# Optimization experiments

Measured on AMD Instinct MI355X. Metric: run time of the kernel, lower is better.

## Reference

```python
import jax, jax.numpy as jnp
import numpy as np

B, IN, H = 8192, 1024, 1024


def setup_inputs() -> dict:
    key = jax.random.key(0)
    ks = jax.random.split(key, 6)
    s = 1.0 / np.sqrt(H)
    return {
        "incoming": jax.random.normal(ks[0], (B, IN), dtype=jnp.float32),
        "state": jax.random.normal(ks[1], (2, B, H), dtype=jnp.float32),
        "Wx": jax.random.normal(ks[2], (4 * H, IN), dtype=jnp.float32) * s,
        "bx": jax.random.normal(ks[3], (4 * H,), dtype=jnp.float32) * s,
        "Wh": jax.random.normal(ks[4], (4 * H, H), dtype=jnp.float32) * s,
        "bh": jax.random.normal(ks[5], (4 * H,), dtype=jnp.float32) * s,
    }


def reference(incoming, state, Wx, bx, Wh, bh):
    # Fused form of 8 Linear layers: gates stacked in (i, f, g, o) order.
    h_prev, c_prev = state[0], state[1]
    gates = (jnp.einsum('bi,gi->bg', incoming, Wx) + bx
             + jnp.einsum('bh,gh->bg', h_prev, Wh) + bh)  # [B, 4H]
    i_g, f_g, g_g, o_g = jnp.split(gates, 4, axis=-1)
    i = jax.nn.sigmoid(i_g)
    f = jax.nn.sigmoid(f_g)
    g = jnp.tanh(g_g)
    o = jax.nn.sigmoid(o_g)
    new_c = f * c_prev + i * g
    new_h = o * jnp.tanh(new_c)
    # output == new_h; return stacked (new_h, new_c) as [2, B, H]
    return jnp.stack([new_h, new_c])
```

## Files before the change

kernel.cpp:

```cpp
#include <hip/hip_runtime.h>
#include <hip/hip_bf16.h>


#define B_DIM 8192
#define H_DIM 1024
#define BH (8192 * 1024)
#define K2 2048

typedef __attribute__((ext_vector_type(4))) float f32x4;
typedef __attribute__((ext_vector_type(8))) __bf16 bf16x8;
typedef __attribute__((ext_vector_type(8))) unsigned short ushort8;

static __device__ __forceinline__ unsigned short f2bf(float f) {
    return __builtin_bit_cast(unsigned short, (__bf16)f);
}
static __device__ __forceinline__ float sigf(float x) {
    return 1.0f / (1.0f + __expf(-x));
}
static __device__ __forceinline__ float tanhft(float x) {
    float e = __expf(2.0f * x);
    return (e - 1.0f) / (e + 1.0f);
}
static __device__ __forceinline__ void gload16(const void* g, void* l) {
    __builtin_amdgcn_global_load_lds(
        (const __attribute__((address_space(1))) unsigned int*)g,
        (__attribute__((address_space(3))) unsigned int*)l, 16, 0, 0);
}
static __device__ __forceinline__ ushort8 cvt8(const float* src) {
    const float4 u = ((const float4*)src)[0];
    const float4 v = ((const float4*)src)[1];
    ushort8 o;
    o[0] = f2bf(u.x); o[1] = f2bf(u.y); o[2] = f2bf(u.z); o[3] = f2bf(u.w);
    o[4] = f2bf(v.x); o[5] = f2bf(v.y); o[6] = f2bf(v.z); o[7] = f2bf(v.w);
    return o;
}

__global__ __launch_bounds__(256) void conv_kernel(
    const float* __restrict__ x, const float* __restrict__ h,
    const float* __restrict__ Wx, const float* __restrict__ Wh,
    unsigned short* __restrict__ A, unsigned short* __restrict__ W)
{
    const int bidx = blockIdx.x;
    if (bidx < 8192) {
        const int id = bidx * 256 + threadIdx.x;
        const int base = id * 8;
        const int b = base >> 11;
        const int k = base & 2047;
        const float* src = (k < 1024) ? (x + (size_t)b * 1024 + k)
                                      : (h + (size_t)b * 1024 + (k - 1024));
        *(ushort8*)(A + base) = cvt8(src);
    } else {
        const int id = (bidx - 8192) * 256 + threadIdx.x;
        const int base = id * 8;
        const int n = base >> 11;
        const int k = base & 2047;
        const int jb = n >> 8, wn = (n >> 6) & 3, g = (n >> 4) & 3, jj = n & 15;
        const int srow = (g << 10) + (jb << 6) + (wn << 4) + jj;
        const float* src = (k < 1024) ? (Wx + (size_t)srow * 1024 + k)
                                      : (Wh + (size_t)srow * 1024 + (k - 1024));
        *(ushort8*)(W + base) = cvt8(src);
    }
}

__global__ __launch_bounds__(512, 2) void lstm_gemm8(
    const unsigned short* __restrict__ Abf, const unsigned short* __restrict__ Wbf,
    const float* __restrict__ bx, const float* __restrict__ bh,
    const float* __restrict__ cprev, float* __restrict__ out)
{
    extern __shared__ unsigned short lds[];

    const int tid = threadIdx.x;
    const int lane = tid & 63;
    const int wv = tid >> 6;
    const int wm = wv >> 2;
    const int wn = wv & 3;
    const int q = lane >> 4, c = lane & 15;

    const int bid = blockIdx.x;
    const int xcd = bid & 7;
    const int idx = bid >> 3;
    const int jb  = xcd * 2 + (idx & 1);
    const int bb  = idx >> 1;
    const int b0 = bb * 256;

    const unsigned short* Ab = Abf + (size_t)b0 * K2;
    const unsigned short* Wb = Wbf + (size_t)(jb * 256) * K2;

    const size_t ssg = (size_t)(tid >> 3) * K2
                     + (size_t)(((tid & 7) ^ ((tid >> 3) & 7)) * 8);
    const unsigned sbase = (unsigned)(tid & 448) * 8;

    const unsigned arow = (unsigned)(wm * 128 + c) * 64;
    const unsigned brow = 16384u + (unsigned)(wn * 64 + c) * 64;
    const unsigned cach = (unsigned)((q ^ (c & 7)) << 3);

    f32x4 acc[8][4];
#pragma unroll
    for (int m = 0; m < 8; ++m)
#pragma unroll
        for (int g = 0; g < 4; ++g) acc[m][g] = f32x4{0.f, 0.f, 0.f, 0.f};

    bf16x8 av[4], bv[4];

#define STG(BUF, ISB, QA, T) do {                                              \
    const unsigned short* _s = (ISB) ? Wb : Ab;                                \
    gload16(_s + ssg + (size_t)(QA) * 64 * K2 + (size_t)((T) & 31) * 64,       \
            &lds[(BUF) * 32768 + (ISB) * 16384 + (QA) * 4096 + sbase]);        \
} while (0)

#define LOADA(BUF, KS, MH) do {                                                \
    const unsigned short* _p = lds + (BUF) * 32768 + (MH) * 4096 + arow        \
                             + (cach ^ ((KS) * 32));                           \
    av[0] = *(const bf16x8*)(_p);                                              \
    av[1] = *(const bf16x8*)(_p + 1024);                                       \
    av[2] = *(const bf16x8*)(_p + 2048);                                       \
    av[3] = *(const bf16x8*)(_p + 3072);                                       \
} while (0)

#define LOADB(BUF, KS) do {                                                    \
    const unsigned short* _p = lds + (BUF) * 32768 + brow                      \
                             + (cach ^ ((KS) * 32));                           \
    bv[0] = *(const bf16x8*)(_p);                                              \
    bv[1] = *(const bf16x8*)(_p + 1024);                                       \
    bv[2] = *(const bf16x8*)(_p + 2048);                                       \
    bv[3] = *(const bf16x8*)(_p + 3072);                                       \
} while (0)

#define MFMA16(MH) do {                                                        \
    __builtin_amdgcn_s_setprio(1);                                             \
    _Pragma("unroll")                                                          \
    for (int _i = 0; _i < 4; ++_i)                                             \
        _Pragma("unroll")                                                      \
        for (int _g = 0; _g < 4; ++_g)                                         \
            acc[(MH) * 4 + _i][_g] = __builtin_amdgcn_mfma_f32_16x16x32_bf16(  \
                av[_i], bv[_g], acc[(MH) * 4 + _i][_g], 0, 0, 0);              \
    __builtin_amdgcn_s_setprio(0);                                             \
} while (0)

#define BAR()    __builtin_amdgcn_s_barrier()
#define WLGKM0() asm volatile("s_waitcnt lgkmcnt(0)")
#define WVM2()   asm volatile("s_waitcnt vmcnt(2)" ::: "memory")

#define TILE(BUF, T1) do {                                                     \
    LOADA(BUF, 0, 0); LOADB(BUF, 0);                                           \
    STG((BUF) ^ 1, 1, 0, T1); STG((BUF) ^ 1, 1, 1, T1);                        \
    BAR(); WLGKM0(); MFMA16(0); WVM2(); BAR();                                 \
    LOADA(BUF, 0, 1);                                                          \
    STG((BUF) ^ 1, 1, 2, T1); STG((BUF) ^ 1, 1, 3, T1);                        \
    BAR(); WLGKM0(); MFMA16(1); BAR();                                         \
    LOADA(BUF, 1, 0); LOADB(BUF, 1);                                           \
    STG((BUF) ^ 1, 0, 0, T1); STG((BUF) ^ 1, 0, 2, T1);                        \
    BAR(); WLGKM0(); MFMA16(0); BAR();                                         \
    LOADA(BUF, 1, 1);                                                          \
    STG((BUF) ^ 1, 0, 1, T1); STG((BUF) ^ 1, 0, 3, T1);                        \
    BAR(); WLGKM0(); MFMA16(1); WVM2(); BAR();                                 \
} while (0)

    STG(0, 1, 0, 0); STG(0, 1, 1, 0); STG(0, 1, 2, 0); STG(0, 1, 3, 0);
    STG(0, 0, 0, 0); STG(0, 0, 2, 0); STG(0, 0, 1, 0); STG(0, 0, 3, 0);
    WVM2();
    BAR();

    for (int u = 0; u < 32; u += 2) {
        TILE(0, u + 1);
        TILE(1, u + 2);
    }

#undef TILE
#undef STG
#undef LOADA
#undef LOADB
#undef MFMA16

    const int j = jb * 64 + wn * 16 + c;
    const float bI = bx[j] + bh[j];
    const float bF = bx[1024 + j] + bh[1024 + j];
    const float bG = bx[2048 + j] + bh[2048 + j];
    const float bO = bx[3072 + j] + bh[3072 + j];
#pragma unroll
    for (int mt = 0; mt < 8; ++mt) {
#pragma unroll
        for (int rr = 0; rr < 4; ++rr) {
            const int row = b0 + wm * 128 + mt * 16 + q * 4 + rr;
            const size_t off = (size_t)row * 1024 + j;
            const float iv = sigf(acc[mt][0][rr] + bI);
            const float fv = sigf(acc[mt][1][rr] + bF);
            const float gv = tanhft(acc[mt][2][rr] + bG);
            const float ov = sigf(acc[mt][3][rr] + bO);
            const float cp = cprev[off];
            const float nc = fv * cp + iv * gv;
            out[off] = ov * tanhft(nc);
            out[BH + off] = nc;
        }
    }
}

__global__ __launch_bounds__(256) void lstm_fallback(
    const float* __restrict__ incoming, const float* __restrict__ state,
    const float* __restrict__ Wx, const float* __restrict__ bx,
    const float* __restrict__ Wh, const float* __restrict__ bh,
    float* __restrict__ out)
{
    __shared__ unsigned short lA[128 * 64];
    __shared__ unsigned short lW[128 * 64];
    const int t = threadIdx.x;
    const int lane = t & 63;
    const int wv = t >> 6;
    const int q = lane >> 4;
    const int c = lane & 15;
    const int j0 = blockIdx.x * 32;
    const int b0 = blockIdx.y * 128;
    const float* hprev = state;
    const float* cprev = state + (size_t)BH;

    f32x4 acc[2][8];
#pragma unroll
    for (int mt = 0; mt < 2; ++mt)
#pragma unroll
        for (int nt = 0; nt < 8; ++nt)
            acc[mt][nt] = f32x4{0.f, 0.f, 0.f, 0.f};

    const int sr = t >> 3;
    const int sk8 = t & 7;

    for (int it = 0; it < 32; ++it) {
        const bool first = (it < 16);
        const float* As = first ? incoming : hprev;
        const float* Ws = first ? Wx : Wh;
        const int kk = first ? it * 64 : it * 64 - 1024;
#pragma unroll
        for (int i = 0; i < 4; ++i) {
            const int r = i * 32 + sr;
            *(ushort8*)&lA[r * 64 + ((sk8 ^ (r & 7)) * 8)] =
                cvt8(As + (size_t)(b0 + r) * 1024 + kk + sk8 * 8);
        }
#pragma unroll
        for (int i = 0; i < 4; ++i) {
            const int n = i * 32 + sr;
            const int grow = ((n >> 5) << 10) + j0 + (n & 31);
            *(ushort8*)&lW[n * 64 + ((sk8 ^ (n & 7)) * 8)] =
                cvt8(Ws + (size_t)grow * 1024 + kk + sk8 * 8);
        }
        __syncthreads();
#pragma unroll
        for (int ks = 0; ks < 2; ++ks) {
            const int k8a = ks * 4 + q;
            bf16x8 av[2], bv[8];
#pragma unroll
            for (int mt = 0; mt < 2; ++mt) {
                const int r = wv * 32 + mt * 16 + c;
                av[mt] = *(const bf16x8*)&lA[r * 64 + ((k8a ^ (r & 7)) * 8)];
            }
#pragma unroll
            for (int nt = 0; nt < 8; ++nt) {
                const int n = nt * 16 + c;
                bv[nt] = *(const bf16x8*)&lW[n * 64 + ((k8a ^ (n & 7)) * 8)];
            }
#pragma unroll
            for (int mt = 0; mt < 2; ++mt)
#pragma unroll
                for (int nt = 0; nt < 8; ++nt)
                    acc[mt][nt] = __builtin_amdgcn_mfma_f32_16x16x32_bf16(
                        av[mt], bv[nt], acc[mt][nt], 0, 0, 0);
        }
        __syncthreads();
    }

    const int b0r = b0 + wv * 32;
#pragma unroll
    for (int jt = 0; jt < 2; ++jt) {
        const int j = j0 + jt * 16 + c;
        const float bI = bx[j] + bh[j];
        const float bF = bx[1024 + j] + bh[1024 + j];
        const float bG = bx[2048 + j] + bh[2048 + j];
        const float bO = bx[3072 + j] + bh[3072 + j];
#pragma unroll
        for (int mt = 0; mt < 2; ++mt) {
#pragma unroll
            for (int rr = 0; rr < 4; ++rr) {
                const int row = b0r + mt * 16 + q * 4 + rr;
                const size_t off = (size_t)row * 1024 + j;
                const float iv = sigf(acc[mt][0 + jt][rr] + bI);
                const float fv = sigf(acc[mt][2 + jt][rr] + bF);
                const float gv = tanhft(acc[mt][4 + jt][rr] + bG);
                const float ov = sigf(acc[mt][6 + jt][rr] + bO);
                const float cp = cprev[off];
                const float nc = fv * cp + iv * gv;
                out[off] = ov * tanhft(nc);
                out[BH + off] = nc;
            }
        }
    }
}

extern "C" void kernel_launch(void* const* d_in, const int* in_sizes, int n_in,
                              void* d_out, int out_size, void* d_ws, size_t ws_size,
                              hipStream_t stream) {
    const float* incoming = (const float*)d_in[0];
    const float* state    = (const float*)d_in[1];
    const float* Wx       = (const float*)d_in[2];
    const float* bx       = (const float*)d_in[3];
    const float* Wh       = (const float*)d_in[4];
    const float* bh       = (const float*)d_in[5];
    float* out = (float*)d_out;

    const float* hprev = state;
    const float* cprev = state + (size_t)BH;

    const size_t A_bytes = (size_t)B_DIM * K2 * 2;
    const size_t W_bytes = (size_t)4 * H_DIM * K2 * 2;

    if (ws_size >= A_bytes + W_bytes) {
        unsigned short* Abf = (unsigned short*)d_ws;
        unsigned short* Wbf = (unsigned short*)((char*)d_ws + A_bytes);
        conv_kernel<<<dim3(12288), dim3(256), 0, stream>>>(
            incoming, hprev, Wx, Wh, Abf, Wbf);
        (void)hipFuncSetAttribute((const void*)lstm_gemm8,
                                  hipFuncAttributeMaxDynamicSharedMemorySize, 131072);
        lstm_gemm8<<<dim3(512), dim3(512), 131072, stream>>>(
            Abf, Wbf, bx, bh, cprev, out);
    } else {
        dim3 grid(H_DIM / 32, B_DIM / 128);
        lstm_fallback<<<grid, dim3(256), 0, stream>>>(
            incoming, state, Wx, bx, Wh, bh, out);
    }
}
```

Before: 159.2 us.

## Restructure LSTM GEMM to 1024-thread blocks with shallower K tiles

The fused bf16 GEMM goes from 512 to 1024 threads per block, and each wave now holds a 64x64 accumulator tile instead of 128x64. The K step shrinks from 64 to 32, which halves LDS use to 64 KB. The four-phase interleaved staging and MFMA schedule is replaced by a simple double-buffered loop that issues the next tile's loads, runs the MFMAs, then waits on all outstanding loads and syncs once per step. This aims for more resident waves and fewer barriers per step. The cost is twice as many K iterations, each with a full vmcnt(0) wait that can expose global-load latency.

Measured after the change: 165.0 us. +3.7%, slower.

```diff
diff --git a/kernel.cpp b/kernel.cpp
--- a/kernel.cpp
+++ b/kernel.cpp
@@ -62,7 +62,7 @@
     }
 }
 
-__global__ __launch_bounds__(512, 2) void lstm_gemm8(
+__global__ __launch_bounds__(1024, 4) void lstm_gemm8(
     const unsigned short* __restrict__ Abf, const unsigned short* __restrict__ Wbf,
     const float* __restrict__ bx, const float* __restrict__ bh,
     const float* __restrict__ cprev, float* __restrict__ out)
@@ -86,90 +86,76 @@
     const unsigned short* Ab = Abf + (size_t)b0 * K2;
     const unsigned short* Wb = Wbf + (size_t)(jb * 256) * K2;
 
-    const size_t ssg = (size_t)(tid >> 3) * K2
-                     + (size_t)(((tid & 7) ^ ((tid >> 3) & 7)) * 8);
-    const unsigned sbase = (unsigned)(tid & 448) * 8;
-
-    const unsigned arow = (unsigned)(wm * 128 + c) * 64;
-    const unsigned brow = 16384u + (unsigned)(wn * 64 + c) * 64;
-    const unsigned cach = (unsigned)((q ^ (c & 7)) << 3);
-
-    f32x4 acc[8][4];
-#pragma unroll
-    for (int m = 0; m < 8; ++m)
+    const size_t ssg = (size_t)(tid >> 2) * K2
+                     + (size_t)(((tid & 3) ^ ((tid >> 3) & 3)) * 8);
+    const unsigned sdst = (unsigned)(tid & 960) * 8;
+
+    const unsigned cq = (unsigned)((q ^ ((c >> 1) & 3)) << 3);
+    const unsigned arow = (unsigned)(wm * 64 + c) * 32 + cq;
+    const unsigned brow = 8192u + (unsigned)(wn * 64 + c) * 32 + cq;
+
+    f32x4 acc[4][4];
+#pragma unroll
+    for (int m = 0; m < 4; ++m)
 #pragma unroll
         for (int g = 0; g < 4; ++g) acc[m][g] = f32x4{0.f, 0.f, 0.f, 0.f};
 
     bf16x8 av[4], bv[4];
 
-#define STG(BUF, ISB, QA, T) do {                                              \
+#define STG(BUF, ISB, T) do {                                                  \
     const unsigned short* _s = (ISB) ? Wb : Ab;                                \
-    gload16(_s + ssg + (size_t)(QA) * 64 * K2 + (size_t)((T) & 31) * 64,       \
-            &lds[(BUF) * 32768 + (ISB) * 16384 + (QA) * 4096 + sbase]);        \
+    gload16(_s + ssg + (size_t)((T) & 63) * 32,                                \
+            &lds[(BUF) * 16384 + (ISB) * 8192 + sdst]);                        \
 } while (0)
 
-#define LOADA(BUF, KS, MH) do {                                                \
-    const unsigned short* _p = lds + (BUF) * 32768 + (MH) * 4096 + arow        \
-                             + (cach ^ ((KS) * 32));                           \
-    av[0] = *(const bf16x8*)(_p);                                              \
-    av[1] = *(const bf16x8*)(_p + 1024);                                       \
-    av[2] = *(const bf16x8*)(_p + 2048);                                       \
-    av[3] = *(const bf16x8*)(_p + 3072);                                       \
+#define RD(BUF) do {                                                           \
+    const unsigned short* _pa = lds + (BUF) * 16384 + arow;                    \
+    const unsigned short* _pb = lds + (BUF) * 16384 + brow;                    \
+    av[0] = *(const bf16x8*)(_pa);                                             \
+    av[1] = *(const bf16x8*)(_pa + 512);                                       \
+    av[2] = *(const bf16x8*)(_pa + 1024);                                      \
+    av[3] = *(const bf16x8*)(_pa + 1536);                                      \
+    bv[0] = *(const bf16x8*)(_pb);                                             \
+    bv[1] = *(const bf16x8*)(_pb + 512);                                       \
+    bv[2] = *(const bf16x8*)(_pb + 1024);                                      \
+    bv[3] = *(const bf16x8*)(_pb + 1536);                                      \
 } while (0)
 
-#define LOADB(BUF, KS) do {                                                    \
-    const unsigned short* _p = lds + (BUF) * 32768 + brow                      \
-                             + (cach ^ ((KS) * 32));                           \
-    bv[0] = *(const bf16x8*)(_p);                                              \
-    bv[1] = *(const bf16x8*)(_p + 1024);                                       \
-    bv[2] = *(const bf16x8*)(_p + 2048);                                       \
-    bv[3] = *(const bf16x8*)(_p + 3072);                                       \
-} while (0)
-
-#define MFMA16(MH) do {                                                        \
+#define MFMA16() do {                                                          \
     __builtin_amdgcn_s_setprio(1);                                             \
     _Pragma("unroll")                                                          \
     for (int _i = 0; _i < 4; ++_i)                                             \
         _Pragma("unroll")                                                      \
         for (int _g = 0; _g < 4; ++_g)                                         \
-            acc[(MH) * 4 + _i][_g] = __builtin_amdgcn_mfma_f32_16x16x32_bf16(  \
-                av[_i], bv[_g], acc[(MH) * 4 + _i][_g], 0, 0, 0);              \
+            acc[_i][_g] = __builtin_amdgcn_mfma_f32_16x16x32_bf16(             \
+                av[_i], bv[_g], acc[_i][_g], 0, 0, 0);                         \
     __builtin_amdgcn_s_setprio(0);                                             \
 } while (0)
 
-#define BAR()    __builtin_amdgcn_s_barrier()
-#define WLGKM0() asm volatile("s_waitcnt lgkmcnt(0)")
-#define WVM2()   asm volatile("s_waitcnt vmcnt(2)" ::: "memory")
-
-#define TILE(BUF, T1) do {                                                     \
-    LOADA(BUF, 0, 0); LOADB(BUF, 0);                                           \
-    STG((BUF) ^ 1, 1, 0, T1); STG((BUF) ^ 1, 1, 1, T1);                        \
-    BAR(); WLGKM0(); MFMA16(0); WVM2(); BAR();                                 \
-    LOADA(BUF, 0, 1);                                                          \
-    STG((BUF) ^ 1, 1, 2, T1); STG((BUF) ^ 1, 1, 3, T1);                        \
-    BAR(); WLGKM0(); MFMA16(1); BAR();                                         \
-    LOADA(BUF, 1, 0); LOADB(BUF, 1);                                           \
-    STG((BUF) ^ 1, 0, 0, T1); STG((BUF) ^ 1, 0, 2, T1);                        \
-    BAR(); WLGKM0(); MFMA16(0); BAR();                                         \
-    LOADA(BUF, 1, 1);                                                          \
-    STG((BUF) ^ 1, 0, 1, T1); STG((BUF) ^ 1, 0, 3, T1);                        \
-    BAR(); WLGKM0(); MFMA16(1); WVM2(); BAR();                                 \
+#define BAR()  __builtin_amdgcn_s_barrier()
+#define WVM0() asm volatile("s_waitcnt vmcnt(0)" ::: "memory")
+
+#define KTILE(BUF, T1) do {                                                    \
+    STG((BUF) ^ 1, 0, T1);                                                     \
+    STG((BUF) ^ 1, 1, T1);                                                     \
+    RD(BUF);                                                                   \
+    MFMA16();                                                                  \
+    WVM0();                                                                    \
+    BAR();                                                                     \
 } while (0)
 
-    STG(0, 1, 0, 0); STG(0, 1, 1, 0); STG(0, 1, 2, 0); STG(0, 1, 3, 0);
-    STG(0, 0, 0, 0); STG(0, 0, 2, 0); STG(0, 0, 1, 0); STG(0, 0, 3, 0);
-    WVM2();
+    STG(0, 0, 0); STG(0, 1, 0);
+    WVM0();
     BAR();
 
-    for (int u = 0; u < 32; u += 2) {
-        TILE(0, u + 1);
-        TILE(1, u + 2);
-    }
-
-#undef TILE
+    for (int t = 0; t < 64; t += 2) {
+        KTILE(0, t + 1);
+        KTILE(1, t + 2);
+    }
+
+#undef KTILE
 #undef STG
-#undef LOADA
-#undef LOADB
+#undef RD
 #undef MFMA16
 
     const int j = jb * 64 + wn * 16 + c;
@@ -178,10 +164,10 @@
     const float bG = bx[2048 + j] + bh[2048 + j];
     const float bO = bx[3072 + j] + bh[3072 + j];
 #pragma unroll
-    for (int mt = 0; mt < 8; ++mt) {
+    for (int mt = 0; mt < 4; ++mt) {
 #pragma unroll
         for (int rr = 0; rr < 4; ++rr) {
-            const int row = b0 + wm * 128 + mt * 16 + q * 4 + rr;
+            const int row = b0 + wm * 64 + mt * 16 + q * 4 + rr;
             const size_t off = (size_t)row * 1024 + j;
             const float iv = sigf(acc[mt][0][rr] + bI);
             const float fv = sigf(acc[mt][1][rr] + bF);
@@ -316,8 +302,8 @@
         conv_kernel<<<dim3(12288), dim3(256), 0, stream>>>(
             incoming, hprev, Wx, Wh, Abf, Wbf);
         (void)hipFuncSetAttribute((const void*)lstm_gemm8,
-                                  hipFuncAttributeMaxDynamicSharedMemorySize, 131072);
-        lstm_gemm8<<<dim3(512), dim3(512), 131072, stream>>>(
+                                  hipFuncAttributeMaxDynamicSharedMemorySize, 65536);
+        lstm_gemm8<<<dim3(512), dim3(1024), 65536, stream>>>(
             Abf, Wbf, bx, bh, cprev, out);
     } else {
         dim3 grid(H_DIM / 32, B_DIM / 128);
```
